# Kernel optimization log

Hardware: AMD Instinct MI355X
Metric: run time of the kernel (lower is better)

The kernel has to match this reference:

```python
import jax, jax.numpy as jnp
import numpy as np

B, S, D_MODEL, N_HEADS, D_FF = 4, 2048, 1024, 16, 4096
HEAD_DIM = D_MODEL // N_HEADS
NUM_BUCKETS, MAX_DISTANCE = 32, 128
EPS = 1e-6


def _relative_position_bucket(relative_position, num_buckets=NUM_BUCKETS, max_distance=MAX_DISTANCE):
    # bidirectional (encoder) variant, matching T5RelativePositionBias
    n = -relative_position
    nb = num_buckets // 2
    ret = (n < 0).astype(jnp.int32) * nb
    n = jnp.abs(n)
    max_exact = nb // 2
    val_if_large = max_exact + (
        jnp.log(jnp.maximum(n, 1).astype(jnp.float32) / max_exact)
        / np.log(max_distance / max_exact) * (nb - max_exact)
    ).astype(jnp.int32)
    val_if_large = jnp.minimum(val_if_large, nb - 1)
    return ret + jnp.where(n < max_exact, n, val_if_large)


def t5_position_bias(rel_emb, q_len, k_len):
    ctx = jnp.arange(q_len)[:, None]
    mem = jnp.arange(k_len)[None, :]
    rp_bucket = _relative_position_bucket(mem - ctx)          # [S, S]
    bias = rel_emb[rp_bucket]                                  # [S, S, H]
    return jnp.transpose(bias, (2, 0, 1))[None]                # [1, H, S, S]


def layer_norm(x, g, b):
    mu = jnp.mean(x, axis=-1, keepdims=True)
    var = jnp.mean(jnp.square(x - mu), axis=-1, keepdims=True)
    return (x - mu) * jax.lax.rsqrt(var + EPS) * g + b


def setup_inputs() -> dict:
    key = jax.random.key(0)
    ks = jax.random.split(key, 20)
    s = 0.02
    p = {
        'src': jax.random.normal(ks[0], (B, S, D_MODEL), jnp.float32),
        'wq': jax.random.normal(ks[1], (D_MODEL, D_MODEL), jnp.float32) * s,
        'bq': jnp.zeros((D_MODEL,), jnp.float32),
        'wk': jax.random.normal(ks[2], (D_MODEL, D_MODEL), jnp.float32) * s,
        'bk': jnp.zeros((D_MODEL,), jnp.float32),
        'wv': jax.random.normal(ks[3], (D_MODEL, D_MODEL), jnp.float32) * s,
        'bv': jnp.zeros((D_MODEL,), jnp.float32),
        'wo': jax.random.normal(ks[4], (D_MODEL, D_MODEL), jnp.float32) * s,
        'bo': jnp.zeros((D_MODEL,), jnp.float32),
        'w1': jax.random.normal(ks[5], (D_MODEL, D_FF), jnp.float32) * s,
        'b1': jnp.zeros((D_FF,), jnp.float32),
        'w2': jax.random.normal(ks[6], (D_FF, D_MODEL), jnp.float32) * s,
        'b2': jnp.zeros((D_MODEL,), jnp.float32),
        'ln1_g': jnp.ones((D_MODEL,), jnp.float32),
        'ln1_b': jnp.zeros((D_MODEL,), jnp.float32),
        'ln2_g': jnp.ones((D_MODEL,), jnp.float32),
        'ln2_b': jnp.zeros((D_MODEL,), jnp.float32),
        'rel_emb': jax.random.normal(ks[7], (NUM_BUCKETS, N_HEADS), jnp.float32) * s,
    }
    return p


def reference(src, wq, bq, wk, bk, wv, bv, wo, bo, w1, b1, w2, b2,
              ln1_g, ln1_b, ln2_g, ln2_b, rel_emb):
    b, s, _ = src.shape

    # --- self-attention block (pre-norm) ---
    xn = layer_norm(src, ln1_g, ln1_b)
    q = (xn @ wq + bq).reshape(b, s, N_HEADS, HEAD_DIM).transpose(0, 2, 1, 3)
    k = (xn @ wk + bk).reshape(b, s, N_HEADS, HEAD_DIM).transpose(0, 2, 1, 3)
    v = (xn @ wv + bv).reshape(b, s, N_HEADS, HEAD_DIM).transpose(0, 2, 1, 3)

    bias = t5_position_bias(rel_emb, s, s)                       # [1,H,S,S]
    scores = jnp.einsum('bhqd,bhkd->bhqk', q, k) / np.sqrt(HEAD_DIM) + bias
    attn = jax.nn.softmax(scores, axis=-1)
    ctx = jnp.einsum('bhqk,bhkd->bhqd', attn, v)                 # [B,H,S,Dh]
    ctx = ctx.transpose(0, 2, 1, 3).reshape(b, s, D_MODEL)
    x = src + (ctx @ wo + bo)

    # --- FFN block (pre-norm, ReLU) ---
    yn = layer_norm(x, ln2_g, ln2_b)
    y = jax.nn.relu(yn @ w1 + b1) @ w2 + b2
    return x + y
```

## Files before the change

### kernel.cpp

```cpp
#include <hip/hip_runtime.h>
#include <math.h>

typedef unsigned short u16;

#define S_LEN 2048
#define BSZ 4
#define DM 1024
#define NH 16
#define HD 64
#define DFF 4096
#define ROWS (BSZ * S_LEN)
#define LOG2E 1.4426950408889634f

typedef __attribute__((__ext_vector_type__(8))) __bf16 bf16x8;
typedef __attribute__((__ext_vector_type__(8))) short short8;
typedef __attribute__((__ext_vector_type__(4))) short short4v;
typedef __attribute__((__ext_vector_type__(4))) float f32x4;
typedef __attribute__((__ext_vector_type__(4))) float float4v;

__device__ __forceinline__ float bf2f(u16 u) {
    union { unsigned int i; float f; } c; c.i = ((unsigned int)u) << 16; return c.f;
}
__device__ __forceinline__ u16 f2bf(float f) {
    union { float f; unsigned int i; } c; c.f = f;
    unsigned int r = c.i + 0x7fffu + ((c.i >> 16) & 1u);
    return (u16)(r >> 16);
}
__device__ __forceinline__ u16 f2bf_cvt(float f) {
    __bf16 h = (__bf16)f;
    return __builtin_bit_cast(u16, h);
}
__device__ __forceinline__ float ldin(const void* p, long i, int f32) {
    return f32 ? ((const float*)p)[i] : bf2f(((const u16*)p)[i]);
}
__device__ __forceinline__ int dtype_f32(const u16* ln1g) {
    return ln1g[0] != 0x3F80;
}
__device__ __forceinline__ void gl_lds16(const void* g, void* l) {
    __builtin_amdgcn_global_load_lds(
        (const __attribute__((address_space(1))) unsigned int*)g,
        (__attribute__((address_space(3))) unsigned int*)l, 16, 0, 0);
}

#define BARR  asm volatile("s_barrier" ::: "memory")
#define LGKM0 asm volatile("s_waitcnt lgkmcnt(0)" ::: "memory")
#define VM4   asm volatile("s_waitcnt vmcnt(4)" ::: "memory")
#define VM2   asm volatile("s_waitcnt vmcnt(2)" ::: "memory")
#define VM0   asm volatile("s_waitcnt vmcnt(0)" ::: "memory")

__device__ __forceinline__ void tr_tile(
    const void* __restrict__ src, u16* __restrict__ dst, int N, int K,
    int bx, int by, int f32, int tid, u16 (*t)[72])
{
#pragma unroll
    for (int i = 0; i < 2; i++) {
        int c = tid + i * 256;
        int row = c >> 3, col = (c & 7) * 8;
        long off = (long)(by * 64 + row) * N + bx * 64 + col;
        short8 v;
        if (f32) {
            const float* s = (const float*)src + off;
            float4v a = *(const float4v*)s;
            float4v b = *(const float4v*)(s + 4);
#pragma unroll
            for (int k = 0; k < 4; k++) { v[k] = (short)f2bf(a[k]); v[k + 4] = (short)f2bf(b[k]); }
        } else {
            v = *(const short8*)((const u16*)src + off);
        }
        *(short8*)(&t[row][col]) = v;
    }
    __syncthreads();
#pragma unroll
    for (int i = 0; i < 2; i++) {
        int c = tid + i * 256;
        int row = c >> 3, col = (c & 7) * 8;
        short8 v;
#pragma unroll
        for (int jj = 0; jj < 8; jj++) v[jj] = (short)t[col + jj][row];
        *(short8*)(dst + (long)(bx * 64 + row) * K + by * 64 + col) = v;
    }
}

__global__ __launch_bounds__(256) void prep_all(
    const void* wq, const void* wk, const void* wv, const void* wo,
    const void* w1, const void* w2,
    const void* bq, const void* bk, const void* bv, const void* bo,
    const void* b1, const void* b2, const void* l1g, const void* l1b,
    const void* l2g, const void* l2b, const void* rel,
    const void* src, u16* __restrict__ xn,
    u16* __restrict__ wqkvt, u16* __restrict__ wot,
    u16* __restrict__ w1t, u16* __restrict__ w2t,
    u16* __restrict__ smalls, float* __restrict__ bias_full)
{
    __shared__ u16 t[64][72];
    __shared__ float ps1[4], ps2[4];
    int z = blockIdx.z;
    int f32 = dtype_f32((const u16*)l1g);

    if (z < 4) {
        if (blockIdx.x >= 16) return;
        const void* s = (z == 0) ? wq : (z == 1) ? wk : (z == 2) ? wv : wo;
        u16* dst = (z < 3) ? wqkvt + (long)z * 1024 * 1024 : wot;
        tr_tile(s, dst, DM, DM, blockIdx.x, blockIdx.y, f32, threadIdx.x, t);
        return;
    }
    if (z == 4) {
        tr_tile(w1, w1t, DFF, DM, blockIdx.x, blockIdx.y, f32, threadIdx.x, t);
        return;
    }
    if (z == 5) {
        tr_tile(w2, w2t, DM, DFF, blockIdx.y, blockIdx.x, f32, threadIdx.x, t);
        return;
    }
    if (z == 6) {
        int bidx = blockIdx.y * 64 + blockIdx.x;
        if (bidx >= 256) return;
        int tid = bidx * 256 + threadIdx.x;
        if (tid < 13312) {
            float v;
            if      (tid < 1024)  v = ldin(bq,  tid,         f32);
            else if (tid < 2048)  v = ldin(bk,  tid - 1024,  f32);
            else if (tid < 3072)  v = ldin(bv,  tid - 2048,  f32);
            else if (tid < 4096)  v = ldin(bo,  tid - 3072,  f32);
            else if (tid < 8192)  v = ldin(b1,  tid - 4096,  f32);
            else if (tid < 9216)  v = ldin(b2,  tid - 8192,  f32);
            else if (tid < 10240) v = ldin(l1g, tid - 9216,  f32);
            else if (tid < 11264) v = ldin(l1b, tid - 10240, f32);
            else if (tid < 12288) v = ldin(l2g, tid - 11264, f32);
            else                  v = ldin(l2b, tid - 12288, f32);
            smalls[tid] = f2bf(v);
        }
        if (tid < 4095 * 16) {
            int dIdx = tid >> 4;
            int h = tid & 15;
            int delta = dIdx - 2047;
            int n = -delta;
            int ret = (n < 0) ? 16 : 0;
            int na = (n < 0) ? -n : n;
            int bkt;
            if (na < 8) {
                bkt = na;
            } else {
                float tval = logf((float)na * 0.125f) * 2.8853900817779268f;
                int v = 8 + (int)tval;
                bkt = v < 15 ? v : 15;
            }
            bkt += ret;
            bias_full[h * 4095 + dIdx] = ldin(rel, bkt * 16 + h, f32) * LOG2E;
        }
        return;
    }
    {
        int row = (z - 7) * 1024 + blockIdx.y * 64 + blockIdx.x;
        int tid = threadIdx.x;
        float vals[4];
        if (f32) {
            float4v v = *(const float4v*)((const float*)src + (long)row * DM + tid * 4);
#pragma unroll
            for (int k = 0; k < 4; k++) vals[k] = v[k];
        } else {
            short4v v = *(const short4v*)((const u16*)src + (long)row * DM + tid * 4);
#pragma unroll
            for (int k = 0; k < 4; k++) vals[k] = bf2f((u16)v[k]);
        }
        float s1 = 0.f, s2 = 0.f;
#pragma unroll
        for (int k = 0; k < 4; k++) { s1 += vals[k]; s2 += vals[k] * vals[k]; }
#pragma unroll
        for (int off = 32; off > 0; off >>= 1) {
            s1 += __shfl_xor(s1, off);
            s2 += __shfl_xor(s2, off);
        }
        int wave = tid >> 6, lane = tid & 63;
        if (lane == 0) { ps1[wave] = s1; ps2[wave] = s2; }
        __syncthreads();
        s1 = ps1[0] + ps1[1] + ps1[2] + ps1[3];
        s2 = ps2[0] + ps2[1] + ps2[2] + ps2[3];
        float mu = s1 * (1.0f / DM);
        float var = s2 * (1.0f / DM) - mu * mu;
        float rs = rsqrtf(var + 1e-6f);
        short4v ov;
#pragma unroll
        for (int k = 0; k < 4; k++) {
            float gv = ldin(l1g, tid * 4 + k, f32);
            float bv = ldin(l1b, tid * 4 + k, f32);
            ov[k] = (short)f2bf((vals[k] - mu) * rs * gv + bv);
        }
        *(short4v*)(xn + (long)row * DM + tid * 4) = ov;
    }
}

__global__ __launch_bounds__(256) void vtrans(
    const u16* __restrict__ v, u16* __restrict__ vt)
{
    __shared__ u16 t[64][72];
    int s0 = blockIdx.x * 64;
    int bh = blockIdx.y;
    const u16* src = v + (long)bh * S_LEN * HD;
    u16* dst = vt + (long)bh * HD * S_LEN;
    int tid = threadIdx.x;
#pragma unroll
    for (int i = 0; i < 2; i++) {
        int c = tid + i * 256;
        int row = c >> 3, col = (c & 7) * 8;
        *(short8*)(&t[row][col]) = *(const short8*)(src + (long)(s0 + row) * HD + col);
    }
    __syncthreads();
#pragma unroll
    for (int i = 0; i < 2; i++) {
        int c = tid + i * 256;
        int row = c >> 3, col = (c & 7) * 8;
        short8 o;
#pragma unroll
        for (int jj = 0; jj < 8; jj++) o[jj] = (short)t[col + jj][row];
        *(short8*)(dst + (long)row * S_LEN + s0 + col) = o;
    }
}

__global__ __launch_bounds__(256) void ln_kernel(
    const void* __restrict__ xin, int external, const u16* __restrict__ ln1g,
    const u16* __restrict__ g, const u16* __restrict__ bta, u16* __restrict__ out)
{
    int f32 = external ? dtype_f32(ln1g) : 0;
    int row = blockIdx.x;
    int tid = threadIdx.x;
    float vals[4];
    if (f32) {
        float4v v = *(const float4v*)((const float*)xin + (long)row * DM + tid * 4);
#pragma unroll
        for (int k = 0; k < 4; k++) vals[k] = v[k];
    } else {
        short4v v = *(const short4v*)((const u16*)xin + (long)row * DM + tid * 4);
#pragma unroll
        for (int k = 0; k < 4; k++) vals[k] = bf2f((u16)v[k]);
    }
    float s1 = 0.f, s2 = 0.f;
#pragma unroll
    for (int k = 0; k < 4; k++) { s1 += vals[k]; s2 += vals[k] * vals[k]; }
#pragma unroll
    for (int off = 32; off > 0; off >>= 1) {
        s1 += __shfl_xor(s1, off);
        s2 += __shfl_xor(s2, off);
    }
    __shared__ float ps1[4], ps2[4];
    int wave = tid >> 6, lane = tid & 63;
    if (lane == 0) { ps1[wave] = s1; ps2[wave] = s2; }
    __syncthreads();
    s1 = ps1[0] + ps1[1] + ps1[2] + ps1[3];
    s2 = ps2[0] + ps2[1] + ps2[2] + ps2[3];
    float mu = s1 * (1.0f / DM);
    float var = s2 * (1.0f / DM) - mu * mu;
    float rs = rsqrtf(var + 1e-6f);
    short4v ov;
#pragma unroll
    for (int k = 0; k < 4; k++) {
        float gv = bf2f(g[tid * 4 + k]);
        float bv = bf2f(bta[tid * 4 + k]);
        ov[k] = (short)f2bf((vals[k] - mu) * rs * gv + bv);
    }
    *(short4v*)(out + (long)row * DM + tid * 4) = ov;
}

#define TM 256
#define TN 256
#define TK 64

#define PHASE(bi, q, STAGE, WAITV)                                             \
    {                                                                          \
        if ((q) == 0) {                                                        \
            _Pragma("unroll")                                                  \
            for (int j = 0; j < 4; j++) {                                      \
                _Pragma("unroll")                                              \
                for (int t = 0; t < 2; t++)                                    \
                    bfr[j][t] = __builtin_bit_cast(bf16x8, *(const short8*)(   \
                        &Bs[bi][wn * 64 + j * 16 + l16][((t * 4 + quad) ^ rxor) * 8])); \
            }                                                                  \
        }                                                                      \
        _Pragma("unroll")                                                      \
        for (int i = 0; i < 2; i++) {                                          \
            _Pragma("unroll")                                                  \
            for (int t = 0; t < 2; t++)                                        \
                af[i][t] = __builtin_bit_cast(bf16x8, *(const short8*)(        \
                    &As[bi][wm * 128 + ((q) * 2 + i) * 16 + l16][((t * 4 + quad) ^ rxor) * 8])); \
        }                                                                      \
        STAGE                                                                  \
        WAITV;                                                                 \
        BARR;                                                                  \
        LGKM0;                                                                 \
        __builtin_amdgcn_sched_barrier(0);                                     \
        __builtin_amdgcn_s_setprio(1);                                         \
        _Pragma("unroll")                                                      \
        for (int i = 0; i < 2; i++) {                                          \
            _Pragma("unroll")                                                  \
            for (int j = 0; j < 4; j++) {                                      \
                acc[(q) * 2 + i][j] = __builtin_amdgcn_mfma_f32_16x16x32_bf16( \
                    af[i][0], bfr[j][0], acc[(q) * 2 + i][j], 0, 0, 0);        \
                acc[(q) * 2 + i][j] = __builtin_amdgcn_mfma_f32_16x16x32_bf16( \
                    af[i][1], bfr[j][1], acc[(q) * 2 + i][j], 0, 0, 0);        \
            }                                                                  \
        }                                                                      \
        __builtin_amdgcn_s_setprio(0);                                         \
        BARR;                                                                  \
    }

__global__ __launch_bounds__(512, 2) void gemm256(
    const u16* __restrict__ A, const u16* __restrict__ Bt,
    const u16* __restrict__ bias, int M, int N, int K, int mode,
    u16* __restrict__ out_q, u16* __restrict__ out_k, u16* __restrict__ out_v,
    u16* __restrict__ outp)
{
    __shared__ u16 As[2][TM][TK];
    __shared__ u16 Bs[2][TN][TK];

    int tid = threadIdx.x;
    int wavei = tid >> 6, lane = tid & 63;
    int quad = lane >> 4, l16 = lane & 15;
    int wm = wavei >> 2, wn = wavei & 3;

    int nwg = gridDim.x * gridDim.y;
    int bid = blockIdx.y * gridDim.x + blockIdx.x;
    int chunk = nwg >> 3;
    int swz = (bid & 7) * chunk + (bid >> 3);
    int bx = swz % gridDim.x, by = swz / gridDim.x;
    long m0 = (long)by * TM, n0 = (long)bx * TN;

    int srow = tid >> 3;
    int pchk = tid & 7;
    int cchk = pchk ^ (srow & 7);
    int rxor = l16 & 7;

    int NT = K / TK;

    auto stageA = [&](int bufi, int h, int t) {
        const u16* g = A + (m0 + h * 128 + srow) * (long)K + (long)t * TK + cchk * 8;
        gl_lds16(g,                 &As[bufi][h * 128 + srow     ][pchk * 8]);
        gl_lds16(g + 64 * (long)K,  &As[bufi][h * 128 + srow + 64][pchk * 8]);
    };
    auto stageB = [&](int bufi, int h, int t) {
        const u16* g = Bt + (n0 + h * 128 + srow) * (long)K + (long)t * TK + cchk * 8;
        gl_lds16(g,                 &Bs[bufi][h * 128 + srow     ][pchk * 8]);
        gl_lds16(g + 64 * (long)K,  &Bs[bufi][h * 128 + srow + 64][pchk * 8]);
    };

    f32x4 acc[8][4];
    f32x4 z = {0.f, 0.f, 0.f, 0.f};
#pragma unroll
    for (int i = 0; i < 8; i++)
#pragma unroll
        for (int j = 0; j < 4; j++) acc[i][j] = z;

    bf16x8 bfr[4][2];
    bf16x8 af[2][2];

    stageA(0, 0, 0); stageA(0, 1, 0); stageB(0, 0, 0); stageB(0, 1, 0);
    stageB(1, 0, 1); stageB(1, 1, 1);
    VM4;
    BARR;

    for (int kt = 0; kt < NT - 2; kt += 2) {
        PHASE(0, 0, { stageA(1, 0, kt + 1); stageA(1, 1, kt + 1); }, (void)0);
        PHASE(0, 1, { stageB(0, 0, kt + 2); }, (void)0);
        PHASE(0, 2, { stageB(0, 1, kt + 2); }, (void)0);
        PHASE(0, 3, {}, VM4);
        PHASE(1, 0, { stageA(0, 0, kt + 2); }, (void)0);
        PHASE(1, 1, { stageA(0, 1, kt + 2); stageB(1, 0, kt + 3); }, (void)0);
        PHASE(1, 2, { stageB(1, 1, kt + 3); }, (void)0);
        PHASE(1, 3, {}, VM4);
    }
    PHASE(0, 0, { stageA(1, 0, NT - 1); stageA(1, 1, NT - 1); }, (void)0);
    PHASE(0, 1, {}, (void)0);
    PHASE(0, 2, {}, (void)0);
    PHASE(0, 3, {}, VM0);
    PHASE(1, 0, {}, (void)0);
    PHASE(1, 1, {}, (void)0);
    PHASE(1, 2, {}, (void)0);
    PHASE(1, 3, {}, (void)0);

#pragma unroll
    for (int i = 0; i < 8; i++) {
#pragma unroll
        for (int j = 0; j < 4; j++) {
#pragma unroll
            for (int r = 0; r < 4; r++) {
                long gr = m0 + wm * 128 + i * 16 + quad * 4 + r;
                long gc = n0 + wn * 64 + j * 16 + l16;
                float val = acc[i][j][r] + bf2f(bias[gc]);
                if (mode == 1) {
                    int sel = (int)(gc >> 10);
                    int cc = (int)(gc & 1023);
                    int h = cc >> 6, d = cc & 63;
                    int b = (int)(gr >> 11), s = (int)(gr & 2047);
                    u16* dst = (sel == 0) ? out_q : (sel == 1 ? out_k : out_v);
                    dst[(((long)(b * NH + h)) * S_LEN + s) * HD + d] = f2bf_cvt(val);
                } else {
                    outp[gr * (long)N + gc] = f2bf_cvt(val > 0.f ? val : 0.f);
                }
            }
        }
    }
}

#define NBM 256
#define NBN 128

#define PHN(bi, half, STAGE, WAITV)                                            \
    {                                                                          \
        if ((half) == 0) {                                                     \
            _Pragma("unroll")                                                  \
            for (int j = 0; j < 2; j++) {                                      \
                _Pragma("unroll")                                              \
                for (int t = 0; t < 2; t++)                                    \
                    nbfr[j][t] = __builtin_bit_cast(bf16x8, *(const short8*)(  \
                        &Bs[bi][wn * 32 + j * 16 + l16][((t * 4 + quad) ^ rxor) * 8])); \
            }                                                                  \
        }                                                                      \
        _Pragma("unroll")                                                      \
        for (int i = 0; i < 4; i++) {                                          \
            _Pragma("unroll")                                                  \
            for (int t = 0; t < 2; t++)                                        \
                naf[i][t] = __builtin_bit_cast(bf16x8, *(const short8*)(       \
                    &As[bi][wm * 128 + ((half) * 4 + i) * 16 + l16][((t * 4 + quad) ^ rxor) * 8])); \
        }                                                                      \
        STAGE                                                                  \
        WAITV;                                                                 \
        BARR;                                                                  \
        LGKM0;                                                                 \
        __builtin_amdgcn_sched_barrier(0);                                     \
        __builtin_amdgcn_s_setprio(1);                                         \
        _Pragma("unroll")                                                      \
        for (int i = 0; i < 4; i++) {                                          \
            _Pragma("unroll")                                                  \
            for (int j = 0; j < 2; j++) {                                      \
                acc[(half) * 4 + i][j] = __builtin_amdgcn_mfma_f32_16x16x32_bf16( \
                    naf[i][0], nbfr[j][0], acc[(half) * 4 + i][j], 0, 0, 0);   \
                acc[(half) * 4 + i][j] = __builtin_amdgcn_mfma_f32_16x16x32_bf16( \
                    naf[i][1], nbfr[j][1], acc[(half) * 4 + i][j], 0, 0, 0);   \
            }                                                                  \
        }                                                                      \
        __builtin_amdgcn_s_setprio(0);                                         \
        BARR;                                                                  \
    }

__global__ __launch_bounds__(512, 2) void gemm256n(
    const u16* __restrict__ A, const u16* __restrict__ Bt,
    const u16* __restrict__ bias, int M, int N, int K, int mode,
    u16* __restrict__ out_q, u16* __restrict__ out_k, u16* __restrict__ out_v,
    const void* __restrict__ res, void* __restrict__ outp,
    const u16* __restrict__ ln1g)
{
    __shared__ u16 As[2][NBM][TK];
    __shared__ u16 Bs[2][NBN][TK];

    int tid = threadIdx.x;
    int wavei = tid >> 6, lane = tid & 63;
    int quad = lane >> 4, l16 = lane & 15;
    int wm = wavei >> 2, wn = wavei & 3;

    int nwg = gridDim.x * gridDim.y;
    int bid = blockIdx.y * gridDim.x + blockIdx.x;
    int chunk = nwg >> 3;
    int swz = (bid & 7) * chunk + (bid >> 3);
    int bx = swz % gridDim.x, by = swz / gridDim.x;
    long m0 = (long)by * NBM, n0 = (long)bx * NBN;
    int flg = (mode == 2 || mode == 4) ? dtype_f32(ln1g) : 0;

    int srow = tid >> 3;
    int pchk = tid & 7;
    int cchk = pchk ^ (srow & 7);
    int rxor = l16 & 7;

    int NT = K / TK;

    auto stageA = [&](int bufi, int h, int t) {
        const u16* g = A + (m0 + h * 128 + srow) * (long)K + (long)t * TK + cchk * 8;
        gl_lds16(g,                 &As[bufi][h * 128 + srow     ][pchk * 8]);
        gl_lds16(g + 64 * (long)K,  &As[bufi][h * 128 + srow + 64][pchk * 8]);
    };
    auto stageB = [&](int bufi, int t) {
        const u16* g = Bt + (n0 + srow) * (long)K + (long)t * TK + cchk * 8;
        gl_lds16(g,                 &Bs[bufi][srow     ][pchk * 8]);
        gl_lds16(g + 64 * (long)K,  &Bs[bufi][srow + 64][pchk * 8]);
    };

    f32x4 acc[8][2];
    f32x4 z = {0.f, 0.f, 0.f, 0.f};
#pragma unroll
    for (int i = 0; i < 8; i++)
#pragma unroll
        for (int j = 0; j < 2; j++) acc[i][j] = z;

    bf16x8 nbfr[2][2];
    bf16x8 naf[4][2];

    stageA(0, 0, 0); stageA(0, 1, 0); stageB(0, 0);
    stageB(1, 1);
    VM2;
    BARR;

    for (int kt = 0; kt < NT - 2; kt += 2) {
        PHN(0, 0, { stageA(1, 0, kt + 1); stageA(1, 1, kt + 1); }, (void)0);
        PHN(0, 1, { stageB(0, kt + 2); }, VM2);
        PHN(1, 0, { stageA(0, 0, kt + 2); stageA(0, 1, kt + 2); }, (void)0);
        PHN(1, 1, { stageB(1, kt + 3); }, VM2);
    }
    PHN(0, 0, { stageA(1, 0, NT - 1); stageA(1, 1, NT - 1); }, (void)0);
    PHN(0, 1, {}, VM0);
    PHN(1, 0, {}, (void)0);
    PHN(1, 1, {}, (void)0);

#pragma unroll
    for (int i = 0; i < 8; i++) {
#pragma unroll
        for (int j = 0; j < 2; j++) {
#pragma unroll
            for (int r = 0; r < 4; r++) {
                long gr = m0 + wm * 128 + i * 16 + quad * 4 + r;
                long gc = n0 + wn * 32 + j * 16 + l16;
                float val = acc[i][j][r] + bf2f(bias[gc]);
                if (mode == 1) {
                    int sel = (int)(gc >> 10);
                    int cc = (int)(gc & 1023);
                    int h = cc >> 6, d = cc & 63;
                    int b = (int)(gr >> 11), s = (int)(gr & 2047);
                    u16* dst = (sel == 0) ? out_q : (sel == 1 ? out_k : out_v);
                    dst[(((long)(b * NH + h)) * S_LEN + s) * HD + d] = f2bf_cvt(val);
                } else if (mode == 2) {
                    long idx = gr * (long)N + gc;
                    float rv = flg ? ((const float*)res)[idx]
                                   : bf2f(((const u16*)res)[idx]);
                    ((u16*)outp)[idx] = f2bf_cvt(val + rv);
                } else {
                    long idx = gr * (long)N + gc;
                    float o = val + bf2f(((const u16*)res)[idx]);
                    if (flg) ((float*)outp)[idx] = o;
                    else     ((u16*)outp)[idx]  = f2bf_cvt(o);
                }
            }
        }
    }
}

__global__ __launch_bounds__(512, 4) void attn_kernel(
    const u16* __restrict__ Qg, const u16* __restrict__ Kg, const u16* __restrict__ Vtg,
    const float* __restrict__ bias_full, u16* __restrict__ ctx)
{
    __shared__ u16 Ks[64][64];
    __shared__ u16 Vt[64][64];
    __shared__ u16 Ps[128][76];
    __shared__ u16 bias_s[2176];

    int nwg = gridDim.x * gridDim.y;
    int bid = blockIdx.y * gridDim.x + blockIdx.x;
    int chunk = nwg >> 3;
    int swz = (bid & 7) * chunk + (bid >> 3);
    int qt = swz % gridDim.x, bh = swz / gridDim.x;

    int b = bh >> 4, h = bh & 15;
    int q0 = qt * 128;
    const u16* Q  = Qg  + (long)bh * S_LEN * HD;
    const u16* Kp = Kg  + (long)bh * S_LEN * HD;
    const u16* Vp = Vtg + (long)bh * HD * S_LEN;

    int tid = threadIdx.x;
    int wave = tid >> 6, lane = tid & 63;
    int quad = lane >> 4, l16 = lane & 15;

    for (int i = tid; i < 2176; i += 512)
        bias_s[i] = f2bf(bias_full[h * 4095 + 1920 + i - q0]);
    float Bneg = bias_full[h * 4095 + 0];
    float Bpos = bias_full[h * 4095 + 4094];

    int isv = wave >= 4;
    int t2 = tid & 255;
    int prow = t2 >> 3, pchk = t2 & 7;
    int cchk = pchk ^ (prow & 7);
    int rxor = l16 & 7;
    int rc0 = (quad ^ rxor) * 8;
    int rc1 = ((4 + quad) ^ rxor) * 8;

    bf16x8 aq[2];
#pragma unroll
    for (int t = 0; t < 2; t++)
        aq[t] = __builtin_bit_cast(bf16x8,
            *(const short8*)(Q + (long)(q0 + wave * 16 + l16) * HD + t * 32 + quad * 8));

    bf16x8 ones;
#pragma unroll
    for (int i = 0; i < 8; i++) ones[i] = (__bf16)1.0f;

    f32x4 o[4];
    f32x4 z = {0.f, 0.f, 0.f, 0.f};
#pragma unroll
    for (int j = 0; j < 4; j++) o[j] = z;
    f32x4 lacc = z;

    int ib = 127 + quad * 4 - wave * 16 - l16;
    const float c0 = 0.125f * LOG2E;

    auto compute = [&](int t0) {
        f32x4 s_[4];
#pragma unroll
        for (int j = 0; j < 4; j++) {
            f32x4 a = z;
            bf16x8 kf0 = __builtin_bit_cast(bf16x8, *(const short8*)(&Ks[j * 16 + l16][rc0]));
            a = __builtin_amdgcn_mfma_f32_16x16x32_bf16(kf0, aq[0], a, 0, 0, 0);
            bf16x8 kf1 = __builtin_bit_cast(bf16x8, *(const short8*)(&Ks[j * 16 + l16][rc1]));
            a = __builtin_amdgcn_mfma_f32_16x16x32_bf16(kf1, aq[1], a, 0, 0, 0);
            s_[j] = a;
        }
        int d0 = t0 - q0;
        int nearb = (d0 >= -153 && d0 <= 217);
        float bconst = (d0 > 0) ? Bpos : Bneg;
#pragma unroll
        for (int j = 0; j < 4; j++) {
            short4v pk;
#pragma unroll
            for (int r = 0; r < 4; r++) {
                float bl = nearb ? bf2f(bias_s[ib + t0 + j * 16 + r]) : bconst;
                float p = __builtin_amdgcn_exp2f(fmaf(s_[j][r], c0, bl));
                pk[r] = (short)f2bf_cvt(p);
            }
            *(short4v*)(&Ps[wave * 16 + l16][j * 16 + quad * 4]) = pk;
        }
        bf16x8 ap[2];
#pragma unroll
        for (int tt = 0; tt < 2; tt++)
            ap[tt] = __builtin_bit_cast(bf16x8,
                *(const short8*)(&Ps[wave * 16 + l16][tt * 32 + quad * 8]));
        lacc = __builtin_amdgcn_mfma_f32_16x16x32_bf16(ap[0], ones, lacc, 0, 0, 0);
        lacc = __builtin_amdgcn_mfma_f32_16x16x32_bf16(ap[1], ones, lacc, 0, 0, 0);
#pragma unroll
        for (int j = 0; j < 4; j++) {
            f32x4 t = o[j];
            bf16x8 bv0 = __builtin_bit_cast(bf16x8, *(const short8*)(&Vt[j * 16 + l16][rc0]));
            t = __builtin_amdgcn_mfma_f32_16x16x32_bf16(ap[0], bv0, t, 0, 0, 0);
            bf16x8 bv1 = __builtin_bit_cast(bf16x8, *(const short8*)(&Vt[j * 16 + l16][rc1]));
            t = __builtin_amdgcn_mfma_f32_16x16x32_bf16(ap[1], bv1, t, 0, 0, 0);
            o[j] = t;
        }
    };

    auto ld0 = [&](int t) -> short8 {
        return isv ? *(const short8*)(Vp + (long)prow * S_LEN + t + cchk * 8)
                   : *(const short8*)(Kp + (long)(t + prow) * HD + cchk * 8);
    };
    auto ld1 = [&](int t) -> short8 {
        return isv ? *(const short8*)(Vp + (long)(32 + prow) * S_LEN + t + cchk * 8)
                   : *(const short8*)(Kp + (long)(t + 32 + prow) * HD + cchk * 8);
    };
    u16* dst0 = isv ? &Vt[prow][pchk * 8] : &Ks[prow][pchk * 8];
    u16* dst1 = isv ? &Vt[32 + prow][pchk * 8] : &Ks[32 + prow][pchk * 8];

    short8 sa0 = ld0(0), sa1 = ld1(0);
    short8 sb0, sb1;

    for (int t0 = 0; t0 < S_LEN; t0 += 128) {
        if (t0 > 0) BARR;
        VM0;
        *(short8*)dst0 = sa0;
        *(short8*)dst1 = sa1;
        sb0 = ld0(t0 + 64);
        sb1 = ld1(t0 + 64);
        LGKM0; BARR;
        compute(t0);

        BARR;
        VM0;
        *(short8*)dst0 = sb0;
        *(short8*)dst1 = sb1;
        if (t0 + 128 < S_LEN) {
            sa0 = ld0(t0 + 128);
            sa1 = ld1(t0 + 128);
        }
        LGKM0; BARR;
        compute(t0 + 64);
    }

#pragma unroll
    for (int r = 0; r < 4; r++) {
        int qr = wave * 16 + quad * 4 + r;
        float linv = 1.0f / lacc[r];
        long srow2 = (long)(b * S_LEN + q0 + qr);
#pragma unroll
        for (int j = 0; j < 4; j++)
            ctx[srow2 * DM + h * HD + j * 16 + l16] = f2bf_cvt(o[j][r] * linv);
    }
}

extern "C" void kernel_launch(void* const* d_in, const int* in_sizes, int n_in,
                              void* d_out, int out_size, void* d_ws, size_t ws_size,
                              hipStream_t stream)
{
    const void* src  = d_in[0];
    const void* wq   = d_in[1];
    const void* bq   = d_in[2];
    const void* wk   = d_in[3];
    const void* bk   = d_in[4];
    const void* wv   = d_in[5];
    const void* bv   = d_in[6];
    const void* wo   = d_in[7];
    const void* bo   = d_in[8];
    const void* w1   = d_in[9];
    const void* b1   = d_in[10];
    const void* w2   = d_in[11];
    const void* b2   = d_in[12];
    const void* ln1g = d_in[13];
    const void* ln1b = d_in[14];
    const void* ln2g = d_in[15];
    const void* ln2b = d_in[16];
    const void* rel  = d_in[17];
    const u16* l1g16 = (const u16*)ln1g;

    char* ws = (char*)d_ws;
    const long MB = 1L << 20;
    u16*   smalls = (u16*)  (ws);
    float* bfull  = (float*)(ws + 65536);
    u16*   xn     = (u16*)  (ws + 1  * MB);
    u16*   vtg    = (u16*)  (ws + 1  * MB);
    u16*   qws    = (u16*)  (ws + 17 * MB);
    u16*   kws    = (u16*)  (ws + 33 * MB);
    u16*   vws    = (u16*)  (ws + 49 * MB);
    u16*   hbuf   = (u16*)  (ws + 1  * MB);
    u16*   ctx    = (u16*)  (ws + 65 * MB);
    u16*   yn     = (u16*)  (ws + 65 * MB);
    u16*   xbf    = (u16*)  (ws + 81 * MB);
    u16*   wqkvt  = (u16*)  (ws + 97 * MB);
    u16*   wot    = (u16*)  (ws + 103 * MB);
    u16*   w1t    = (u16*)  (ws + 105 * MB);
    u16*   w2t    = (u16*)  (ws + 113 * MB);

    prep_all<<<dim3(64, 16, 15), 256, 0, stream>>>(
        wq, wk, wv, wo, w1, w2, bq, bk, bv, bo, b1, b2,
        ln1g, ln1b, ln2g, ln2b, rel, src, xn,
        wqkvt, wot, w1t, w2t, smalls, bfull);

    gemm256n<<<dim3(3072 / NBN, ROWS / NBM), 512, 0, stream>>>(
        xn, wqkvt, smalls + 0, ROWS, 3072, DM, 1,
        qws, kws, vws, nullptr, nullptr, l1g16);

    vtrans<<<dim3(S_LEN / 64, BSZ * NH), 256, 0, stream>>>(vws, vtg);

    attn_kernel<<<dim3(S_LEN / 128, BSZ * NH), 512, 0, stream>>>(qws, kws, vtg, bfull, ctx);

    gemm256n<<<dim3(DM / NBN, ROWS / NBM), 512, 0, stream>>>(
        ctx, wot, smalls + 3072, ROWS, DM, DM, 2,
        nullptr, nullptr, nullptr, src, xbf, l1g16);

    ln_kernel<<<ROWS, 256, 0, stream>>>(xbf, 0, l1g16,
                                        smalls + 11264, smalls + 12288, yn);

    gemm256<<<dim3(DFF / TN, ROWS / TM), 512, 0, stream>>>(
        yn, w1t, smalls + 4096, ROWS, DFF, DM, 3, nullptr, nullptr, nullptr, hbuf);

    gemm256n<<<dim3(DM / NBN, ROWS / NBM), 512, 0, stream>>>(
        hbuf, w2t, smalls + 8192, ROWS, DM, DFF, 4,
        nullptr, nullptr, nullptr, xbf, d_out, l1g16);
}
```

Before: 562.7 us.

## Fuse V transpose into QKV GEMM epilogue and switch QKV to gemm256

The QKV projection now runs on the gemm256 kernel, whose epilogue writes V directly in transposed [B,H,D,S] layout as packed 4-element stores. The separate vtrans kernel and its extra read and write of V are removed. The QKV GEMM also moves from the 256x128 tile kernel to the larger-tile gemm256, which changes tile shape and occupancy. The transposed stores are strided by S_LEN per lane, which may be less coalesced than the earlier row-major writes.

```diff
diff --git a/kernel.cpp b/kernel.cpp
--- a/kernel.cpp
+++ b/kernel.cpp
@@ -187,33 +187,6 @@
             ov[k] = (short)f2bf((vals[k] - mu) * rs * gv + bv);
         }
         *(short4v*)(xn + (long)row * DM + tid * 4) = ov;
-    }
-}
-
-__global__ __launch_bounds__(256) void vtrans(
-    const u16* __restrict__ v, u16* __restrict__ vt)
-{
-    __shared__ u16 t[64][72];
-    int s0 = blockIdx.x * 64;
-    int bh = blockIdx.y;
-    const u16* src = v + (long)bh * S_LEN * HD;
-    u16* dst = vt + (long)bh * HD * S_LEN;
-    int tid = threadIdx.x;
-#pragma unroll
-    for (int i = 0; i < 2; i++) {
-        int c = tid + i * 256;
-        int row = c >> 3, col = (c & 7) * 8;
-        *(short8*)(&t[row][col]) = *(const short8*)(src + (long)(s0 + row) * HD + col);
-    }
-    __syncthreads();
-#pragma unroll
-    for (int i = 0; i < 2; i++) {
-        int c = tid + i * 256;
-        int row = c >> 3, col = (c & 7) * 8;
-        short8 o;
-#pragma unroll
-        for (int jj = 0; jj < 8; jj++) o[jj] = (short)t[col + jj][row];
-        *(short8*)(dst + (long)row * S_LEN + s0 + col) = o;
     }
 }
 
@@ -380,20 +353,33 @@
     for (int i = 0; i < 8; i++) {
 #pragma unroll
         for (int j = 0; j < 4; j++) {
-#pragma unroll
-            for (int r = 0; r < 4; r++) {
-                long gr = m0 + wm * 128 + i * 16 + quad * 4 + r;
-                long gc = n0 + wn * 64 + j * 16 + l16;
-                float val = acc[i][j][r] + bf2f(bias[gc]);
-                if (mode == 1) {
-                    int sel = (int)(gc >> 10);
-                    int cc = (int)(gc & 1023);
-                    int h = cc >> 6, d = cc & 63;
-                    int b = (int)(gr >> 11), s = (int)(gr & 2047);
-                    u16* dst = (sel == 0) ? out_q : (sel == 1 ? out_k : out_v);
-                    dst[(((long)(b * NH + h)) * S_LEN + s) * HD + d] = f2bf_cvt(val);
+            long gr0 = m0 + wm * 128 + i * 16 + quad * 4;
+            long gc = n0 + wn * 64 + j * 16 + l16;
+            float bsv = bf2f(bias[gc]);
+            if (mode == 1) {
+                int sel = (int)(gc >> 10);
+                int cc = (int)(gc & 1023);
+                int h = cc >> 6, d = cc & 63;
+                int b = (int)(gr0 >> 11), s0 = (int)(gr0 & 2047);
+                if (sel == 2) {
+                    short4v pk;
+#pragma unroll
+                    for (int r = 0; r < 4; r++)
+                        pk[r] = (short)f2bf_cvt(acc[i][j][r] + bsv);
+                    *(short4v*)(out_v +
+                        (((long)(b * NH + h)) * HD + d) * S_LEN + s0) = pk;
                 } else {
-                    outp[gr * (long)N + gc] = f2bf_cvt(val > 0.f ? val : 0.f);
+                    u16* dst = (sel == 0) ? out_q : out_k;
+#pragma unroll
+                    for (int r = 0; r < 4; r++)
+                        dst[(((long)(b * NH + h)) * S_LEN + s0 + r) * HD + d] =
+                            f2bf_cvt(acc[i][j][r] + bsv);
+                }
+            } else {
+#pragma unroll
+                for (int r = 0; r < 4; r++) {
+                    float val = acc[i][j][r] + bsv;
+                    outp[(gr0 + r) * (long)N + gc] = f2bf_cvt(val > 0.f ? val : 0.f);
                 }
             }
         }
@@ -444,7 +430,6 @@
 __global__ __launch_bounds__(512, 2) void gemm256n(
     const u16* __restrict__ A, const u16* __restrict__ Bt,
     const u16* __restrict__ bias, int M, int N, int K, int mode,
-    u16* __restrict__ out_q, u16* __restrict__ out_k, u16* __restrict__ out_v,
     const void* __restrict__ res, void* __restrict__ outp,
     const u16* __restrict__ ln1g)
 {
@@ -462,7 +447,7 @@
     int swz = (bid & 7) * chunk + (bid >> 3);
     int bx = swz % gridDim.x, by = swz / gridDim.x;
     long m0 = (long)by * NBM, n0 = (long)bx * NBN;
-    int flg = (mode == 2 || mode == 4) ? dtype_f32(ln1g) : 0;
+    int flg = dtype_f32(ln1g);
 
     int srow = tid >> 3;
     int pchk = tid & 7;
@@ -517,20 +502,12 @@
                 long gr = m0 + wm * 128 + i * 16 + quad * 4 + r;
                 long gc = n0 + wn * 32 + j * 16 + l16;
                 float val = acc[i][j][r] + bf2f(bias[gc]);
-                if (mode == 1) {
-                    int sel = (int)(gc >> 10);
-                    int cc = (int)(gc & 1023);
-                    int h = cc >> 6, d = cc & 63;
-                    int b = (int)(gr >> 11), s = (int)(gr & 2047);
-                    u16* dst = (sel == 0) ? out_q : (sel == 1 ? out_k : out_v);
-                    dst[(((long)(b * NH + h)) * S_LEN + s) * HD + d] = f2bf_cvt(val);
-                } else if (mode == 2) {
-                    long idx = gr * (long)N + gc;
+                long idx = gr * (long)N + gc;
+                if (mode == 2) {
                     float rv = flg ? ((const float*)res)[idx]
                                    : bf2f(((const u16*)res)[idx]);
                     ((u16*)outp)[idx] = f2bf_cvt(val + rv);
                 } else {
-                    long idx = gr * (long)N + gc;
                     float o = val + bf2f(((const u16*)res)[idx]);
                     if (flg) ((float*)outp)[idx] = o;
                     else     ((u16*)outp)[idx]  = f2bf_cvt(o);
@@ -716,10 +693,9 @@
     u16*   smalls = (u16*)  (ws);
     float* bfull  = (float*)(ws + 65536);
     u16*   xn     = (u16*)  (ws + 1  * MB);
-    u16*   vtg    = (u16*)  (ws + 1  * MB);
     u16*   qws    = (u16*)  (ws + 17 * MB);
     u16*   kws    = (u16*)  (ws + 33 * MB);
-    u16*   vws    = (u16*)  (ws + 49 * MB);
+    u16*   vtg    = (u16*)  (ws + 49 * MB);
     u16*   hbuf   = (u16*)  (ws + 1  * MB);
     u16*   ctx    = (u16*)  (ws + 65 * MB);
     u16*   yn     = (u16*)  (ws + 65 * MB);
@@ -734,17 +710,13 @@
         ln1g, ln1b, ln2g, ln2b, rel, src, xn,
         wqkvt, wot, w1t, w2t, smalls, bfull);
 
-    gemm256n<<<dim3(3072 / NBN, ROWS / NBM), 512, 0, stream>>>(
-        xn, wqkvt, smalls + 0, ROWS, 3072, DM, 1,
-        qws, kws, vws, nullptr, nullptr, l1g16);
-
-    vtrans<<<dim3(S_LEN / 64, BSZ * NH), 256, 0, stream>>>(vws, vtg);
+    gemm256<<<dim3(3072 / TN, ROWS / TM), 512, 0, stream>>>(
+        xn, wqkvt, smalls + 0, ROWS, 3072, DM, 1, qws, kws, vtg, nullptr);
 
     attn_kernel<<<dim3(S_LEN / 128, BSZ * NH), 512, 0, stream>>>(qws, kws, vtg, bfull, ctx);
 
     gemm256n<<<dim3(DM / NBN, ROWS / NBM), 512, 0, stream>>>(
-        ctx, wot, smalls + 3072, ROWS, DM, DM, 2,
-        nullptr, nullptr, nullptr, src, xbf, l1g16);
+        ctx, wot, smalls + 3072, ROWS, DM, DM, 2, src, xbf, l1g16);
 
     ln_kernel<<<ROWS, 256, 0, stream>>>(xbf, 0, l1g16,
                                         smalls + 11264, smalls + 12288, yn);
@@ -753,6 +725,5 @@
         yn, w1t, smalls + 4096, ROWS, DFF, DM, 3, nullptr, nullptr, nullptr, hbuf);
 
     gemm256n<<<dim3(DM / NBN, ROWS / NBM), 512, 0, stream>>>(
-        hbuf, w2t, smalls + 8192, ROWS, DM, DFF, 4,
-        nullptr, nullptr, nullptr, xbf, d_out, l1g16);
-}
+        hbuf, w2t, smalls + 8192, ROWS, DM, DFF, 4, xbf, d_out, l1g16);
+}
```

New measurement: 544.6 us. 3.2% less time.
